# Optimization experiments

Hardware: AMD Instinct MI355X
Metric: run time of the kernel (lower is better)

The kernel has to match this reference:

```python
import jax, jax.numpy as jnp
import numpy as np

D = 256; DFFN = 1024; H = 8; NLVL = 4; NPNT = 4; HD = D // H
BS = 4; NQ = 100; NPTS = 25
SPATIAL = [(128, 128), (64, 64), (32, 32), (16, 16)]
LEN_IN = sum(h * w for h, w in SPATIAL)


def _ln(x, g, b, eps=1e-5):
    m = x.mean(-1, keepdims=True)
    v = ((x - m) ** 2).mean(-1, keepdims=True)
    return (x - m) * jax.lax.rsqrt(v + eps) * g + b


def _mha(q, k, v, w_in, b_in, w_out, b_out):
    # torch nn.MultiheadAttention math, batch-first layout [B,S,D]
    B, Sq, _ = q.shape; Sk = k.shape[1]
    wq, wk, wv = jnp.split(w_in, 3, 0); bq, bk, bv = jnp.split(b_in, 3)
    qh = (q @ wq.T + bq).reshape(B, Sq, H, HD).transpose(0, 2, 1, 3)
    kh = (k @ wk.T + bk).reshape(B, Sk, H, HD).transpose(0, 2, 1, 3)
    vh = (v @ wv.T + bv).reshape(B, Sk, H, HD).transpose(0, 2, 1, 3)
    a = jax.nn.softmax(jnp.einsum('bhqd,bhkd->bhqk', qh, kh) * (1.0 / float(np.sqrt(HD))), -1)
    o = jnp.einsum('bhqk,bhkd->bhqd', a, vh).transpose(0, 2, 1, 3).reshape(B, Sq, D)
    return o @ w_out.T + b_out


def _msdeform(query, ref, src, off_w, off_b, aw_w, aw_b, val_w, val_b, out_w, out_b):
    # MSDeformAttn: per-query multi-level bilinear sampling + weighted aggregation
    bs, Lq, _ = query.shape
    value = (src @ val_w.T + val_b).reshape(bs, LEN_IN, H, HD)
    off = (query @ off_w.T + off_b).reshape(bs, Lq, H, NLVL, NPNT, 2)
    aw = jax.nn.softmax((query @ aw_w.T + aw_b).reshape(bs, Lq, H, NLVL * NPNT), -1)
    aw = aw.reshape(bs, Lq, H, NLVL, NPNT)
    norm = jnp.array([[w, h] for h, w in SPATIAL], jnp.float32)  # (W,H) per level
    loc = ref[:, :, None, :, None, :] + off / norm[None, None, None, :, None, :]
    out = jnp.zeros((bs, H, Lq, HD), query.dtype)
    start = 0
    for l, (hh, ww) in enumerate(SPATIAL):
        v_l = value[:, start:start + hh * ww].transpose(0, 2, 1, 3)  # [bs,H,hw,HD]
        start += hh * ww
        # grid_sample align_corners=False pixel coords: loc*size - 0.5
        x = (loc[:, :, :, l, :, 0] * ww - 0.5).transpose(0, 2, 1, 3).reshape(bs, H, Lq * NPNT)
        y = (loc[:, :, :, l, :, 1] * hh - 0.5).transpose(0, 2, 1, 3).reshape(bs, H, Lq * NPNT)
        x0 = jnp.floor(x); y0 = jnp.floor(y); wx = x - x0; wy = y - y0
        x0i = x0.astype(jnp.int32); y0i = y0.astype(jnp.int32); x1i = x0i + 1; y1i = y0i + 1
        def g(xi, yi):
            valid = ((xi >= 0) & (xi < ww) & (yi >= 0) & (yi < hh)).astype(query.dtype)
            idx = jnp.clip(yi, 0, hh - 1) * ww + jnp.clip(xi, 0, ww - 1)
            return jnp.take_along_axis(v_l, idx[..., None], axis=2) * valid[..., None]
        s = (g(x0i, y0i) * ((1 - wx) * (1 - wy))[..., None]
             + g(x1i, y0i) * (wx * (1 - wy))[..., None]
             + g(x0i, y1i) * ((1 - wx) * wy)[..., None]
             + g(x1i, y1i) * (wx * wy)[..., None])
        s = s.reshape(bs, H, Lq, NPNT, HD)
        out = out + (s * aw[:, :, :, l].transpose(0, 2, 1, 3)[..., None]).sum(3)
    return out.transpose(0, 2, 1, 3).reshape(bs, Lq, D) @ out_w.T + out_b


def _fwd(tgt, query_pos, reference_points, src,
         w_in_intra, b_in_intra, w_out_intra, b_out_intra, g_norm_intra, b_norm_intra,
         w_in_inter, b_in_inter, w_out_inter, b_out_inter, g_norm_inter, b_norm_inter,
         off_w, off_b, aw_w, aw_b, val_w, val_b, co_w, co_b, g_norm_cross, b_norm_cross,
         lin1_w, lin1_b, lin2_w, lin2_b, g_norm3, b_norm3):
    bs, nq, npts, d = tgt.shape
    # intra-instance self-attention (over control points)
    q = (tgt + query_pos).reshape(bs * nq, npts, d)
    t2 = _mha(q, q, tgt.reshape(bs * nq, npts, d), w_in_intra, b_in_intra, w_out_intra, b_out_intra)
    tgt = _ln(tgt + t2.reshape(bs, nq, npts, d), g_norm_intra, b_norm_intra)
    # inter-instance self-attention (over queries), no pos embed per source code
    ti = tgt.transpose(0, 2, 1, 3).reshape(bs * npts, nq, d)
    t2 = _mha(ti, ti, ti, w_in_inter, b_in_inter, w_out_inter, b_out_inter)
    ti = _ln(ti + t2, g_norm_inter, b_norm_inter).reshape(bs, npts, nq, d).transpose(0, 2, 1, 3)
    # deformable cross-attention
    ref = jnp.broadcast_to(reference_points[:, :, None], (bs, nq, npts, NLVL, 2)).reshape(bs, nq * npts, NLVL, 2)
    qc = (ti + query_pos).reshape(bs, nq * npts, d)
    t2 = _msdeform(qc, ref, src, off_w, off_b, aw_w, aw_b, val_w, val_b, co_w, co_b).reshape(bs, nq, npts, d)
    tgt = _ln(ti + t2, g_norm_cross, b_norm_cross)
    # FFN
    ff = jax.nn.relu(tgt @ lin1_w.T + lin1_b) @ lin2_w.T + lin2_b
    return _ln(tgt + ff, g_norm3, b_norm3)


def setup_inputs() -> dict:
    key = jax.random.key(0)
    ki = iter(jax.random.split(key, 40))
    def rn(shape, sc=0.02):
        return jax.random.normal(next(ki), shape, jnp.float32) * sc
    inp = dict(
        tgt=jax.random.normal(next(ki), (BS, NQ, NPTS, D), jnp.float32),
        query_pos=jax.random.normal(next(ki), (BS, NQ, NPTS, D), jnp.float32),
        reference_points=jax.random.uniform(next(ki), (BS, NQ, NLVL, 2), jnp.float32),
        src=jax.random.normal(next(ki), (BS, LEN_IN, D), jnp.float32),
        w_in_intra=rn((3 * D, D)), b_in_intra=jnp.zeros((3 * D,), jnp.float32),
        w_out_intra=rn((D, D)), b_out_intra=jnp.zeros((D,), jnp.float32),
        g_norm_intra=jnp.ones((D,), jnp.float32), b_norm_intra=jnp.zeros((D,), jnp.float32),
        w_in_inter=rn((3 * D, D)), b_in_inter=jnp.zeros((3 * D,), jnp.float32),
        w_out_inter=rn((D, D)), b_out_inter=jnp.zeros((D,), jnp.float32),
        g_norm_inter=jnp.ones((D,), jnp.float32), b_norm_inter=jnp.zeros((D,), jnp.float32),
        off_w=rn((H * NLVL * NPNT * 2, D), 0.001), off_b=rn((H * NLVL * NPNT * 2,), 0.5),
        aw_w=rn((H * NLVL * NPNT, D)), aw_b=jnp.zeros((H * NLVL * NPNT,), jnp.float32),
        val_w=rn((D, D)), val_b=jnp.zeros((D,), jnp.float32),
        co_w=rn((D, D)), co_b=jnp.zeros((D,), jnp.float32),
        g_norm_cross=jnp.ones((D,), jnp.float32), b_norm_cross=jnp.zeros((D,), jnp.float32),
        lin1_w=rn((DFFN, D)), lin1_b=jnp.zeros((DFFN,), jnp.float32),
        lin2_w=rn((D, DFFN)), lin2_b=jnp.zeros((D,), jnp.float32),
        g_norm3=jnp.ones((D,), jnp.float32), b_norm3=jnp.zeros((D,), jnp.float32),
        src_spatial_shapes=jnp.array(SPATIAL, jnp.int32),
        level_start_index=jnp.array(np.cumsum([0] + [h * w for h, w in SPATIAL[:-1]]), jnp.int32),
    )
    return inp


def reference(tgt, query_pos, reference_points, src,
              w_in_intra, b_in_intra, w_out_intra, b_out_intra, g_norm_intra, b_norm_intra,
              w_in_inter, b_in_inter, w_out_inter, b_out_inter, g_norm_inter, b_norm_inter,
              off_w, off_b, aw_w, aw_b, val_w, val_b, co_w, co_b, g_norm_cross, b_norm_cross,
              lin1_w, lin1_b, lin2_w, lin2_b, g_norm3, b_norm3,
              src_spatial_shapes, level_start_index):
    # spatial shapes / level starts are compile-time constants (SPATIAL); args kept for signature parity
    return _fwd(tgt, query_pos, reference_points, src,
                w_in_intra, b_in_intra, w_out_intra, b_out_intra, g_norm_intra, b_norm_intra,
                w_in_inter, b_in_inter, w_out_inter, b_out_inter, g_norm_inter, b_norm_inter,
                off_w, off_b, aw_w, aw_b, val_w, val_b, co_w, co_b, g_norm_cross, b_norm_cross,
                lin1_w, lin1_b, lin2_w, lin2_b, g_norm3, b_norm3)
```

## Files before the change

### kernel.cpp

```cpp
#include <hip/hip_runtime.h>
#include <math.h>

#define DMODEL 256
#define HEADS  8
#define HDIM   32
#define BS     4
#define NQ     100
#define NPTS   25
#define LQ     2500
#define M10K   10000
#define LEN_IN 21760
#define MVAL   87040

typedef float f32x4 __attribute__((ext_vector_type(4)));
typedef short s16x8 __attribute__((ext_vector_type(8)));
typedef unsigned short u16;

static __device__ __forceinline__ short f2bf(float f) {
    unsigned u = __builtin_bit_cast(unsigned, f);
    u = (u + 0x7fffu + ((u >> 16) & 1u)) >> 16;
    return (short)u;
}
static __device__ __forceinline__ unsigned pack2(float lo, float hi) {
    return (unsigned)(u16)f2bf(lo) | ((unsigned)(u16)f2bf(hi) << 16);
}
static __device__ __forceinline__ float bf_lo(unsigned u) {
    return __builtin_bit_cast(float, u << 16);
}
static __device__ __forceinline__ float bf_hi(unsigned u) {
    return __builtin_bit_cast(float, u & 0xffff0000u);
}

#define LDSK 40

__global__ __launch_bounds__(256) void convert_weights_kernel(
    const float* __restrict__ s0, const float* __restrict__ s1,
    const float* __restrict__ s2, const float* __restrict__ s3,
    const float* __restrict__ s4, const float* __restrict__ s5,
    const float* __restrict__ s6, const float* __restrict__ s7,
    const float* __restrict__ s8, const float* __restrict__ s9,
    u16* __restrict__ dst)
{
    int t8 = (blockIdx.x * 256 + threadIdx.x) * 8;
    if (t8 >= 1277952) return;
    const float* s; int base;
    if      (t8 <  196608) { s = s0; base = 0;       }
    else if (t8 <  262144) { s = s1; base = 196608;  }
    else if (t8 <  458752) { s = s2; base = 262144;  }
    else if (t8 <  524288) { s = s3; base = 458752;  }
    else if (t8 <  589824) { s = s4; base = 524288;  }
    else if (t8 <  622592) { s = s5; base = 589824;  }
    else if (t8 <  688128) { s = s6; base = 622592;  }
    else if (t8 <  753664) { s = s7; base = 688128;  }
    else if (t8 < 1015808) { s = s8; base = 753664;  }
    else                   { s = s9; base = 1015808; }
    const float* p = s + (t8 - base);
    float4 a = *(const float4*)p;
    float4 b = *(const float4*)(p + 4);
    s16x8 v;
    v[0]=f2bf(a.x); v[1]=f2bf(a.y); v[2]=f2bf(a.z); v[3]=f2bf(a.w);
    v[4]=f2bf(b.x); v[5]=f2bf(b.y); v[6]=f2bf(b.z); v[7]=f2bf(b.w);
    *(s16x8*)(dst + t8) = v;
}

__global__ __launch_bounds__(256) void add_convert_kernel(
    const float* __restrict__ a, const float* __restrict__ b,
    u16* __restrict__ xb, u16* __restrict__ ab, int n8)
{
    int i = blockIdx.x * 256 + threadIdx.x;
    if (i >= n8) return;
    size_t o = (size_t)i * 8;
    float4 a0 = *(const float4*)(a + o);
    float4 a1 = *(const float4*)(a + o + 4);
    if (ab) {
        s16x8 v;
        v[0]=f2bf(a0.x); v[1]=f2bf(a0.y); v[2]=f2bf(a0.z); v[3]=f2bf(a0.w);
        v[4]=f2bf(a1.x); v[5]=f2bf(a1.y); v[6]=f2bf(a1.z); v[7]=f2bf(a1.w);
        *(s16x8*)(ab + o) = v;
    }
    if (b) {
        float4 b0 = *(const float4*)(b + o);
        float4 b1 = *(const float4*)(b + o + 4);
        a0.x += b0.x; a0.y += b0.y; a0.z += b0.z; a0.w += b0.w;
        a1.x += b1.x; a1.y += b1.y; a1.z += b1.z; a1.w += b1.w;
    }
    s16x8 v;
    v[0]=f2bf(a0.x); v[1]=f2bf(a0.y); v[2]=f2bf(a0.z); v[3]=f2bf(a0.w);
    v[4]=f2bf(a1.x); v[5]=f2bf(a1.y); v[6]=f2bf(a1.z); v[7]=f2bf(a1.w);
    *(s16x8*)(xb + o) = v;
}

__global__ __launch_bounds__(256) void gemm_mfma_kernel(
    const u16* __restrict__ A, int lda,
    const u16* __restrict__ W, int K,
    const float* __restrict__ bias,
    float* __restrict__ C, int ldc, int M)
{
    __shared__ short As[64 * LDSK];
    __shared__ short Ws[64 * LDSK];

    const int tid = threadIdx.x;
    const int m0 = blockIdx.y * 64, n0 = blockIdx.x * 64;
    const int srow = tid >> 2;
    const int skseg = (tid & 3) * 8;
    const int wave = tid >> 6;
    const int wm = wave & 1, wn = wave >> 1;
    const int lane = tid & 63;
    const int lrow = lane & 15;
    const int kq = lane >> 4;

    f32x4 acc[2][2];
#pragma unroll
    for (int i = 0; i < 2; ++i)
#pragma unroll
        for (int j = 0; j < 2; ++j) acc[i][j] = (f32x4)(0.f);

    for (int k0 = 0; k0 < K; k0 += 32) {
        int gm = m0 + srow;
        s16x8 av = (s16x8)0;
        if (gm < M) av = *(const s16x8*)(A + (size_t)gm * lda + k0 + skseg);
        s16x8 wv = *(const s16x8*)(W + (size_t)(n0 + srow) * K + k0 + skseg);
        *(s16x8*)&As[srow * LDSK + skseg] = av;
        *(s16x8*)&Ws[srow * LDSK + skseg] = wv;
        __syncthreads();

        s16x8 af[2], bfv[2];
#pragma unroll
        for (int i = 0; i < 2; ++i)
            af[i] = *(const s16x8*)&As[(wm * 32 + i * 16 + lrow) * LDSK + kq * 8];
#pragma unroll
        for (int j = 0; j < 2; ++j)
            bfv[j] = *(const s16x8*)&Ws[(wn * 32 + j * 16 + lrow) * LDSK + kq * 8];
#pragma unroll
        for (int i = 0; i < 2; ++i)
#pragma unroll
            for (int j = 0; j < 2; ++j)
                acc[i][j] = __builtin_amdgcn_mfma_f32_16x16x32_bf16(af[i], bfv[j], acc[i][j], 0, 0, 0);
        __syncthreads();
    }

#pragma unroll
    for (int i = 0; i < 2; ++i)
#pragma unroll
        for (int j = 0; j < 2; ++j) {
            int col = n0 + wn * 32 + j * 16 + lrow;
            float bv = bias[col];
#pragma unroll
            for (int reg = 0; reg < 4; ++reg) {
                int gm = m0 + wm * 32 + i * 16 + kq * 4 + reg;
                if (gm < M) C[(size_t)gm * ldc + col] = acc[i][j][reg] + bv;
            }
        }
}

__global__ __launch_bounds__(256) void gemm_mfma128_kernel(
    const u16* __restrict__ A, int lda,
    const u16* __restrict__ W, int K,
    const float* __restrict__ bias,
    void* __restrict__ Cv, int ldc,
    int M, int relu, int out_bf16)
{
    __shared__ short As[128 * LDSK];
    __shared__ short Ws[128 * LDSK];

    const int tid = threadIdx.x;
    const int m0 = blockIdx.y * 128, n0 = blockIdx.x * 128;

    const int srow = tid >> 1;
    const int sk = (tid & 1) * 16;

    const int wave = tid >> 6;
    const int wm = wave & 1, wn = wave >> 1;
    const int lane = tid & 63;
    const int lrow = lane & 15;
    const int kq = lane >> 4;

    f32x4 acc[4][4];
#pragma unroll
    for (int i = 0; i < 4; ++i)
#pragma unroll
        for (int j = 0; j < 4; ++j) acc[i][j] = (f32x4)(0.f);

    for (int k0 = 0; k0 < K; k0 += 32) {
        int gm = m0 + srow;
        s16x8 a0 = (s16x8)0, a1 = (s16x8)0;
        if (gm < M) {
            const u16* ap = A + (size_t)gm * lda + k0 + sk;
            a0 = *(const s16x8*)ap;
            a1 = *(const s16x8*)(ap + 8);
        }
        const u16* wp = W + (size_t)(n0 + srow) * K + k0 + sk;
        s16x8 w0 = *(const s16x8*)wp;
        s16x8 w1 = *(const s16x8*)(wp + 8);
        *(s16x8*)&As[srow * LDSK + sk]     = a0;
        *(s16x8*)&As[srow * LDSK + sk + 8] = a1;
        *(s16x8*)&Ws[srow * LDSK + sk]     = w0;
        *(s16x8*)&Ws[srow * LDSK + sk + 8] = w1;
        __syncthreads();

        s16x8 af[4], bfv[4];
#pragma unroll
        for (int i = 0; i < 4; ++i)
            af[i] = *(const s16x8*)&As[(wm * 64 + i * 16 + lrow) * LDSK + kq * 8];
#pragma unroll
        for (int j = 0; j < 4; ++j)
            bfv[j] = *(const s16x8*)&Ws[(wn * 64 + j * 16 + lrow) * LDSK + kq * 8];
#pragma unroll
        for (int i = 0; i < 4; ++i)
#pragma unroll
            for (int j = 0; j < 4; ++j)
                acc[i][j] = __builtin_amdgcn_mfma_f32_16x16x32_bf16(af[i], bfv[j], acc[i][j], 0, 0, 0);
        __syncthreads();
    }

#pragma unroll
    for (int i = 0; i < 4; ++i)
#pragma unroll
        for (int j = 0; j < 4; ++j) {
            int col = n0 + wn * 64 + j * 16 + lrow;
            float bv = bias[col];
#pragma unroll
            for (int reg = 0; reg < 4; ++reg) {
                int gm = m0 + wm * 64 + i * 16 + kq * 4 + reg;
                if (gm < M) {
                    float v = acc[i][j][reg] + bv;
                    if (relu) v = fmaxf(v, 0.f);
                    if (out_bf16)
                        ((u16*)Cv)[(size_t)gm * ldc + col] = (u16)f2bf(v);
                    else
                        ((float*)Cv)[(size_t)gm * ldc + col] = v;
                }
            }
        }
}

__global__ __launch_bounds__(256) void gemm_value_kernel(
    const float* __restrict__ A,
    const u16* __restrict__ W,
    const float* __restrict__ bias,
    u16* __restrict__ C, int M)
{
    __shared__ short As[64 * LDSK];
    __shared__ short Ws[256 * LDSK];

    const int tid = threadIdx.x;
    const int m0 = blockIdx.x * 64;

    const int arow = tid >> 2;
    const int ak = (tid & 3) * 8;

    const int wave = tid >> 6;
    const int lane = tid & 63;
    const int lrow = lane & 15;
    const int kq = lane >> 4;

    f32x4 acc[4][4];
#pragma unroll
    for (int i = 0; i < 4; ++i)
#pragma unroll
        for (int j = 0; j < 4; ++j) acc[i][j] = (f32x4)(0.f);

    for (int k0 = 0; k0 < 256; k0 += 32) {
        int gm = m0 + arow;
        s16x8 av = (s16x8)0;
        if (gm < M) {
            const float* ap = A + (size_t)gm * 256 + k0 + ak;
            float4 a0 = *(const float4*)ap;
            float4 a1 = *(const float4*)(ap + 4);
            av[0]=f2bf(a0.x); av[1]=f2bf(a0.y); av[2]=f2bf(a0.z); av[3]=f2bf(a0.w);
            av[4]=f2bf(a1.x); av[5]=f2bf(a1.y); av[6]=f2bf(a1.z); av[7]=f2bf(a1.w);
        }
        *(s16x8*)&As[arow * LDSK + ak] = av;
#pragma unroll
        for (int it = 0; it < 4; ++it) {
            int n = (tid >> 2) + it * 64;
            s16x8 wv = *(const s16x8*)(W + (size_t)n * 256 + k0 + ak);
            *(s16x8*)&Ws[n * LDSK + ak] = wv;
        }
        __syncthreads();

        s16x8 af[4], bfv[4];
#pragma unroll
        for (int i = 0; i < 4; ++i)
            af[i] = *(const s16x8*)&As[(i * 16 + lrow) * LDSK + kq * 8];
#pragma unroll
        for (int j = 0; j < 4; ++j)
            bfv[j] = *(const s16x8*)&Ws[(wave * 64 + j * 16 + lrow) * LDSK + kq * 8];
#pragma unroll
        for (int i = 0; i < 4; ++i)
#pragma unroll
            for (int j = 0; j < 4; ++j)
                acc[i][j] = __builtin_amdgcn_mfma_f32_16x16x32_bf16(af[i], bfv[j], acc[i][j], 0, 0, 0);
        __syncthreads();
    }

#pragma unroll
    for (int i = 0; i < 4; ++i)
#pragma unroll
        for (int j = 0; j < 4; ++j) {
            int col = wave * 64 + j * 16 + lrow;
            float bv = bias[col];
#pragma unroll
            for (int reg = 0; reg < 4; ++reg) {
                int gm = m0 + i * 16 + kq * 4 + reg;
                if (gm < M)
                    C[(size_t)gm * 256 + col] = (u16)f2bf(acc[i][j][reg] + bv);
            }
        }
}

__global__ __launch_bounds__(512) void inter_attn_kernel(
    const float* __restrict__ qkv, u16* __restrict__ out, float scale)
{
    __shared__ float4 Kv[100][16];
    __shared__ float4 Ml4[100];
    __shared__ float4 Ll4[100];
    __shared__ float  O[100][33];

    const int b = blockIdx.x, h = blockIdx.y;
    const float* base = qkv + (size_t)b * 100 * 768;
    const int tid = threadIdx.x;
    const int r = tid & 127, kc = tid >> 7;

    for (int idx = tid; idx < 1600; idx += 512) {
        int row = idx >> 4, seg = idx & 15;
        const float* src = (seg < 8)
            ? base + row * 768 + 256 + h * 32 + seg * 4
            : base + row * 768 + 512 + h * 32 + (seg - 8) * 4;
        Kv[row][seg] = *(const float4*)src;
    }
    for (int idx = tid; idx < 100 * 33; idx += 512)
        ((float*)O)[idx] = 0.f;

    float q[32];
    if (r < 100) {
        const float* qp = base + r * 768 + h * 32;
#pragma unroll
        for (int c4 = 0; c4 < 8; ++c4) {
            float4 f = *(const float4*)(qp + c4 * 4);
            q[c4*4+0] = f.x; q[c4*4+1] = f.y; q[c4*4+2] = f.z; q[c4*4+3] = f.w;
        }
    }
    __syncthreads();

    float m = -1e30f, l = 0.f, acc[32];
#pragma unroll
    for (int c = 0; c < 32; ++c) acc[c] = 0.f;

    if (r < 100) {
        const int j0 = kc * 25;
#pragma unroll 2
        for (int s = 0; s < 25; ++s) {
            const float4* kr = &Kv[j0 + s][0];
            float dot = 0.f;
#pragma unroll
            for (int c4 = 0; c4 < 8; ++c4) {
                float4 kf = kr[c4];
                dot = fmaf(q[c4*4+0], kf.x, dot);
                dot = fmaf(q[c4*4+1], kf.y, dot);
                dot = fmaf(q[c4*4+2], kf.z, dot);
                dot = fmaf(q[c4*4+3], kf.w, dot);
            }
            dot *= scale;
            float mn = fmaxf(m, dot);
            float alpha = __expf(m - mn);
            float p = __expf(dot - mn);
            l = l * alpha + p;
            const float4* vr = &Kv[j0 + s][8];
#pragma unroll
            for (int c4 = 0; c4 < 8; ++c4) {
                float4 vf = vr[c4];
                acc[c4*4+0] = acc[c4*4+0] * alpha + p * vf.x;
                acc[c4*4+1] = acc[c4*4+1] * alpha + p * vf.y;
                acc[c4*4+2] = acc[c4*4+2] * alpha + p * vf.z;
                acc[c4*4+3] = acc[c4*4+3] * alpha + p * vf.w;
            }
            m = mn;
        }
        ((float*)&Ml4[r])[kc] = m;
        ((float*)&Ll4[r])[kc] = l;
    }
    __syncthreads();

    float alphaK = 0.f, Ltot = 1.f;
    if (r < 100) {
        float4 mv = Ml4[r];
        float4 lv = Ll4[r];
        float M = fmaxf(fmaxf(mv.x, mv.y), fmaxf(mv.z, mv.w));
        Ltot = __expf(mv.x - M) * lv.x + __expf(mv.y - M) * lv.y
             + __expf(mv.z - M) * lv.z + __expf(mv.w - M) * lv.w;
        alphaK = __expf(m - M);
    }
    for (int cc = 0; cc < 4; ++cc) {
        if (kc == cc && r < 100) {
#pragma unroll
            for (int c = 0; c < 32; ++c) O[r][c] += alphaK * acc[c];
        }
        __syncthreads();
    }
    if (kc == 0 && r < 100) {
        float inv = 1.f / Ltot;
        unsigned* op = (unsigned*)(out + ((size_t)b * 100 + r) * 256 + h * 32);
#pragma unroll
        for (int c = 0; c < 16; ++c)
            op[c] = pack2(O[r][2*c] * inv, O[r][2*c+1] * inv);
    }
}

__global__ __launch_bounds__(256) void intra_attn_kernel(
    const float* __restrict__ qkv, u16* __restrict__ out, float scale)
{
    __shared__ float4 KV[25][128];

    const int b = blockIdx.x;
    const int h = threadIdx.x >> 5, r = threadIdx.x & 31;
    const float* base = qkv + (size_t)b * 25 * 768;

    for (int idx = threadIdx.x; idx < 3200; idx += 256) {
        int row = idx >> 7, c = idx & 127;
        KV[row][c] = *(const float4*)(base + row * 768 + 256 + c * 4);
    }

    float q[32];
    if (r < 25) {
        const float* qp = base + r * 768 + h * 32;
#pragma unroll
        for (int c4 = 0; c4 < 8; ++c4) {
            float4 f = *(const float4*)(qp + c4 * 4);
            q[c4*4+0] = f.x; q[c4*4+1] = f.y; q[c4*4+2] = f.z; q[c4*4+3] = f.w;
        }
    }
    __syncthreads();

    if (r < 25) {
        float m = -1e30f, l = 0.f, acc[32];
#pragma unroll
        for (int c = 0; c < 32; ++c) acc[c] = 0.f;
#pragma unroll 2
        for (int j = 0; j < 25; ++j) {
            const float4* kr = &KV[j][h * 8];
            float dot = 0.f;
#pragma unroll
            for (int c4 = 0; c4 < 8; ++c4) {
                float4 kf = kr[c4];
                dot = fmaf(q[c4*4+0], kf.x, dot);
                dot = fmaf(q[c4*4+1], kf.y, dot);
                dot = fmaf(q[c4*4+2], kf.z, dot);
                dot = fmaf(q[c4*4+3], kf.w, dot);
            }
            dot *= scale;
            float mn = fmaxf(m, dot);
            float alpha = __expf(m - mn);
            float p = __expf(dot - mn);
            l = l * alpha + p;
            const float4* vr = &KV[j][64 + h * 8];
#pragma unroll
            for (int c4 = 0; c4 < 8; ++c4) {
                float4 vf = vr[c4];
                acc[c4*4+0] = acc[c4*4+0] * alpha + p * vf.x;
                acc[c4*4+1] = acc[c4*4+1] * alpha + p * vf.y;
                acc[c4*4+2] = acc[c4*4+2] * alpha + p * vf.z;
                acc[c4*4+3] = acc[c4*4+3] * alpha + p * vf.w;
            }
            m = mn;
        }
        float inv = 1.f / l;
        unsigned* op = (unsigned*)(out + ((size_t)b * 25 + r) * 256 + h * 32);
#pragma unroll
        for (int c = 0; c < 16; ++c)
            op[c] = pack2(acc[2*c] * inv, acc[2*c+1] * inv);
    }
}

__global__ __launch_bounds__(64) void add_ln_kernel(
    const float* __restrict__ a, const float* __restrict__ b,
    const float* __restrict__ g, const float* __restrict__ beta,
    float* __restrict__ out, u16* __restrict__ out_bf, int transpose_mode)
{
    const int r = blockIdx.x;
    const int lane = threadIdx.x;
    const float* ar = a + (size_t)r * 256;
    const float* br = b + (size_t)r * 256;
    float x[4];
    float s = 0.f;
#pragma unroll
    for (int i = 0; i < 4; ++i) {
        x[i] = ar[lane + 64 * i] + br[lane + 64 * i];
        s += x[i];
    }
#pragma unroll
    for (int off = 32; off >= 1; off >>= 1) s += __shfl_xor(s, off);
    float mean = s * (1.f / 256.f);
    float vs = 0.f;
#pragma unroll
    for (int i = 0; i < 4; ++i) { float d = x[i] - mean; vs += d * d; }
#pragma unroll
    for (int off = 32; off >= 1; off >>= 1) vs += __shfl_xor(vs, off);
    float rstd = rsqrtf(vs * (1.f / 256.f) + 1e-5f);

    size_t ro = r;
    if (transpose_mode) {
        int q = r % 100; int bp = r / 100; int p = bp % 25; int bb = bp / 25;
        ro = ((size_t)bb * 100 + q) * 25 + p;
    }
    float* orow = out + ro * 256;
    u16* brow = out_bf ? out_bf + ro * 256 : (u16*)0;
#pragma unroll
    for (int i = 0; i < 4; ++i) {
        int c = lane + 64 * i;
        float v = (x[i] - mean) * rstd * g[c] + beta[c];
        orow[c] = v;
        if (brow) brow[c] = (u16)f2bf(v);
    }
}

__global__ __launch_bounds__(64) void tgt_to_ti_kernel(
    const float* __restrict__ tgt1, float* __restrict__ ti, u16* __restrict__ tib)
{
    const int r = blockIdx.x;
    int q = r % 100; int bp = r / 100; int p = bp % 25; int b = bp / 25;
    const float4* srcp = (const float4*)(tgt1 + (((size_t)b * 100 + q) * 25 + p) * 256);
    float4 v = srcp[threadIdx.x];
    ((float4*)(ti + (size_t)r * 256))[threadIdx.x] = v;
    uint2 pk = make_uint2(pack2(v.x, v.y), pack2(v.z, v.w));
    ((uint2*)(tib + (size_t)r * 256))[threadIdx.x] = pk;
}

__global__ __launch_bounds__(256, 4) void msdeform_sample_kernel(
    const u16* __restrict__ value,
    const float* __restrict__ off,
    const float* __restrict__ awl,
    const float* __restrict__ refp,
    u16* __restrict__ sampled)
{
    const int unit = blockIdx.x * 8 + (threadIdx.x >> 5);
    const int t = threadIdx.x & 31;
    const int h = t >> 2, c8 = t & 3;
    const int b = unit / LQ, lq = unit - b * LQ;
    const int q = lq / NPTS;

    const float* awp = awl + (size_t)unit * 128 + h * 16;
    float w[16];
    float mx = -1e30f;
#pragma unroll
    for (int k = 0; k < 16; ++k) { w[k] = awp[k]; mx = fmaxf(mx, w[k]); }
    float sum = 0.f;
#pragma unroll
    for (int k = 0; k < 16; ++k) { w[k] = __expf(w[k] - mx); sum += w[k]; }
    const float inv = 1.f / sum;

    const float* offp = off + (size_t)unit * 256 + h * 32;
    const float* rp = refp + ((size_t)b * 100 + q) * 8;
    const u16* vbase = value + (size_t)b * LEN_IN * 256 + h * 32 + c8 * 8;

    float acc[8];
#pragma unroll
    for (int k = 0; k < 8; ++k) acc[k] = 0.f;

    int start = 0;
    const int sz[4] = {128, 64, 32, 16};
#pragma unroll
    for (int l = 0; l < 4; ++l) {
        const int hh = sz[l], ww = sz[l];
        const float rx = rp[l * 2 + 0], ry = rp[l * 2 + 1];
#pragma unroll 1
        for (int pt = 0; pt < 4; ++pt) {
            float ox = offp[(l * 4 + pt) * 2 + 0];
            float oy = offp[(l * 4 + pt) * 2 + 1];
            float x = rx * ww + ox - 0.5f;
            float y = ry * hh + oy - 0.5f;
            float x0f = floorf(x), y0f = floorf(y);
            float wx = x - x0f, wy = y - y0f;
            int x0 = (int)x0f, y0 = (int)y0f;
            int x1 = x0 + 1, y1 = y0 + 1;
            float aw = w[l * 4 + pt] * inv;

            int x0c = min(max(x0, 0), ww - 1), x1c = min(max(x1, 0), ww - 1);
            int y0c = min(max(y0, 0), hh - 1), y1c = min(max(y1, 0), hh - 1);
            float w00 = aw * (1.f - wx) * (1.f - wy);
            float w10 = aw * wx * (1.f - wy);
            float w01 = aw * (1.f - wx) * wy;
            float w11 = aw * wx * wy;
            if (!(x0 >= 0 && x0 < ww)) { w00 = 0.f; w01 = 0.f; }
            if (!(x1 >= 0 && x1 < ww)) { w10 = 0.f; w11 = 0.f; }
            if (!(y0 >= 0 && y0 < hh)) { w00 = 0.f; w10 = 0.f; }
            if (!(y1 >= 0 && y1 < hh)) { w01 = 0.f; w11 = 0.f; }

            uint4 u00 = *(const uint4*)(vbase + (size_t)(start + y0c * ww + x0c) * 256);
            uint4 u10 = *(const uint4*)(vbase + (size_t)(start + y0c * ww + x1c) * 256);
            uint4 u01 = *(const uint4*)(vbase + (size_t)(start + y1c * ww + x0c) * 256);
            uint4 u11 = *(const uint4*)(vbase + (size_t)(start + y1c * ww + x1c) * 256);

#define ACC4(u, wgt) \
            acc[0] = fmaf(wgt, bf_lo(u.x), acc[0]); \
            acc[1] = fmaf(wgt, bf_hi(u.x), acc[1]); \
            acc[2] = fmaf(wgt, bf_lo(u.y), acc[2]); \
            acc[3] = fmaf(wgt, bf_hi(u.y), acc[3]); \
            acc[4] = fmaf(wgt, bf_lo(u.z), acc[4]); \
            acc[5] = fmaf(wgt, bf_hi(u.z), acc[5]); \
            acc[6] = fmaf(wgt, bf_lo(u.w), acc[6]); \
            acc[7] = fmaf(wgt, bf_hi(u.w), acc[7]);
            ACC4(u00, w00); ACC4(u10, w10); ACC4(u01, w01); ACC4(u11, w11);
#undef ACC4
        }
        start += hh * ww;
    }

    uint4 pk;
    pk.x = pack2(acc[0], acc[1]); pk.y = pack2(acc[2], acc[3]);
    pk.z = pack2(acc[4], acc[5]); pk.w = pack2(acc[6], acc[7]);
    *(uint4*)(sampled + (size_t)unit * 256 + h * 32 + c8 * 8) = pk;
}

extern "C" void kernel_launch(void* const* d_in, const int* in_sizes, int n_in,
                              void* d_out, int out_size, void* d_ws, size_t ws_size,
                              hipStream_t stream)
{
    (void)in_sizes; (void)n_in; (void)out_size; (void)ws_size;

    const float* tgt        = (const float*)d_in[0];
    const float* query_pos  = (const float*)d_in[1];
    const float* refp       = (const float*)d_in[2];
    const float* src        = (const float*)d_in[3];
    const float* w_in_intra = (const float*)d_in[4];
    const float* b_in_intra = (const float*)d_in[5];
    const float* w_out_intra= (const float*)d_in[6];
    const float* b_out_intra= (const float*)d_in[7];
    const float* g_ln_intra = (const float*)d_in[8];
    const float* b_ln_intra = (const float*)d_in[9];
    const float* w_in_inter = (const float*)d_in[10];
    const float* b_in_inter = (const float*)d_in[11];
    const float* w_out_inter= (const float*)d_in[12];
    const float* b_out_inter= (const float*)d_in[13];
    const float* g_ln_inter = (const float*)d_in[14];
    const float* b_ln_inter = (const float*)d_in[15];
    const float* off_w      = (const float*)d_in[16];
    const float* off_b      = (const float*)d_in[17];
    const float* aw_w       = (const float*)d_in[18];
    const float* aw_b       = (const float*)d_in[19];
    const float* val_w      = (const float*)d_in[20];
    const float* val_b      = (const float*)d_in[21];
    const float* co_w       = (const float*)d_in[22];
    const float* co_b       = (const float*)d_in[23];
    const float* g_ln_cross = (const float*)d_in[24];
    const float* b_ln_cross = (const float*)d_in[25];
    const float* lin1_w     = (const float*)d_in[26];
    const float* lin1_b     = (const float*)d_in[27];
    const float* lin2_w     = (const float*)d_in[28];
    const float* lin2_b     = (const float*)d_in[29];
    const float* g_ln3      = (const float*)d_in[30];
    const float* b_ln3      = (const float*)d_in[31];

    float* ws    = (float*)d_ws;
    float* qkv   = ws;
    float* tmp   = ws + 7680000;
    u16*   attnb = (u16*)(ws + 10240000);
    float* tgt1  = ws + 11520000;
    float* ti    = ws + 14080000;
    u16*   tib   = (u16*)(ws + 16640000);
    float* tA    = ws + 17920000;
    u16*   qcb   = (u16*)(ws + 20480000);
    u16*   x1b   = (u16*)(ws + 21760000);
    u16*   tgtb  = (u16*)(ws + 23040000);
    float* awl   = ws + 24320000;
    u16*   valueb= (u16*)(ws + 25600000);
    u16*   wb    = (u16*)(ws + 36741120);
    float* out   = (float*)d_out;

    u16* wb_in_intra  = wb;
    u16* wb_out_intra = wb + 196608;
    u16* wb_in_inter  = wb + 262144;
    u16* wb_out_inter = wb + 458752;
    u16* wb_off       = wb + 524288;
    u16* wb_aw        = wb + 589824;
    u16* wb_val       = wb + 622592;
    u16* wb_co        = wb + 688128;
    u16* wb_lin1      = wb + 753664;
    u16* wb_lin2      = wb + 1015808;

    const float scale = 0.17677669529663687f;
    const int MB128 = (M10K + 127) / 128;

    convert_weights_kernel<<<624, 256, 0, stream>>>(
        w_in_intra, w_out_intra, w_in_inter, w_out_inter, off_w,
        aw_w, val_w, co_w, lin1_w, lin2_w, wb);
    add_convert_kernel<<<1250, 256, 0, stream>>>(tgt, query_pos, x1b, tgtb, 320000);

    gemm_mfma128_kernel<<<dim3(4, MB128), 256, 0, stream>>>(x1b, 256, wb_in_intra, 256,
                                                            b_in_intra, qkv, 768, M10K, 0, 0);
    gemm_mfma128_kernel<<<dim3(2, MB128), 256, 0, stream>>>(tgtb, 256, wb_in_intra + 512 * 256, 256,
                                                            b_in_intra + 512, qkv + 512, 768, M10K, 0, 0);
    intra_attn_kernel<<<400, 256, 0, stream>>>(qkv, attnb, scale);
    gemm_mfma128_kernel<<<dim3(2, MB128), 256, 0, stream>>>(attnb, 256, wb_out_intra, 256,
                                                            b_out_intra, tmp, 256, M10K, 0, 0);
    add_ln_kernel<<<M10K, 64, 0, stream>>>(tgt, tmp, g_ln_intra, b_ln_intra, tgt1, (u16*)0, 0);

    tgt_to_ti_kernel<<<M10K, 64, 0, stream>>>(tgt1, ti, tib);
    gemm_mfma128_kernel<<<dim3(6, MB128), 256, 0, stream>>>(tib, 256, wb_in_inter, 256,
                                                            b_in_inter, qkv, 768, M10K, 0, 0);
    inter_attn_kernel<<<dim3(100, 8), 512, 0, stream>>>(qkv, attnb, scale);
    gemm_mfma128_kernel<<<dim3(2, MB128), 256, 0, stream>>>(attnb, 256, wb_out_inter, 256,
                                                            b_out_inter, tmp, 256, M10K, 0, 0);
    add_ln_kernel<<<M10K, 64, 0, stream>>>(ti, tmp, g_ln_inter, b_ln_inter, tA, (u16*)0, 1);

    add_convert_kernel<<<1250, 256, 0, stream>>>(tA, query_pos, qcb, (u16*)0, 320000);
    gemm_value_kernel<<<1360, 256, 0, stream>>>(src, wb_val, val_b, valueb, MVAL);
    gemm_mfma128_kernel<<<dim3(2, MB128), 256, 0, stream>>>(qcb, 256, wb_off, 256,
                                                            off_b, tgt1, 256, M10K, 0, 0);
    gemm_mfma_kernel<<<dim3(2, 157), 256, 0, stream>>>(qcb, 256, wb_aw, 256,
                                                       aw_b, awl, 128, M10K);
    msdeform_sample_kernel<<<1250, 256, 0, stream>>>(valueb, tgt1, awl, refp, attnb);
    gemm_mfma128_kernel<<<dim3(2, MB128), 256, 0, stream>>>(attnb, 256, wb_co, 256,
                                                            co_b, tmp, 256, M10K, 0, 0);
    add_ln_kernel<<<M10K, 64, 0, stream>>>(tA, tmp, g_ln_cross, b_ln_cross, ti, tib, 0);

    gemm_mfma128_kernel<<<dim3(8, MB128), 256, 0, stream>>>(tib, 256, wb_lin1, 256,
                                                            lin1_b, valueb, 1024, M10K, 1, 1);
    gemm_mfma128_kernel<<<dim3(2, MB128), 256, 0, stream>>>(valueb, 1024, wb_lin2, 1024,
                                                            lin2_b, tmp, 256, M10K, 0, 0);
    add_ln_kernel<<<M10K, 64, 0, stream>>>(ti, tmp, g_ln3, b_ln3, out, (u16*)0, 0);
}
```

Baseline: 548.0 us.

## Prefetch GEMM tiles to registers, use MFMA inter-attention, smaller tiles for N=256

Adds register double-buffering to all three GEMM kernels, so the global loads for the next K-slice are issued after the barrier and overlap with the MFMA work on the current slice. Replaces the scalar FP32 online-softmax inter-attention kernel with a bf16 MFMA version that computes QK^T, softmax and PV through padded LDS tiles. Switches the N=256 GEMMs from 128x128 to 64x64 tiles to launch more blocks. This gives more parallelism at the cost of extra register pressure and lower per-block reuse, and attention probabilities are now rounded to bf16.

```diff
diff --git a/kernel.cpp b/kernel.cpp
--- a/kernel.cpp
+++ b/kernel.cpp
@@ -94,7 +94,8 @@
     const u16* __restrict__ A, int lda,
     const u16* __restrict__ W, int K,
     const float* __restrict__ bias,
-    float* __restrict__ C, int ldc, int M)
+    void* __restrict__ Cv, int ldc,
+    int M, int relu, int out_bf16)
 {
     __shared__ short As[64 * LDSK];
     __shared__ short Ws[64 * LDSK];
@@ -109,20 +110,28 @@
     const int lrow = lane & 15;
     const int kq = lane >> 4;
 
+    const int gm = m0 + srow;
+    const u16* aptr = A + (size_t)gm * lda + skseg;
+    const u16* wptr = W + (size_t)(n0 + srow) * K + skseg;
+
     f32x4 acc[2][2];
 #pragma unroll
     for (int i = 0; i < 2; ++i)
 #pragma unroll
         for (int j = 0; j < 2; ++j) acc[i][j] = (f32x4)(0.f);
 
+    s16x8 avr = (s16x8)0, wvr;
+    if (gm < M) avr = *(const s16x8*)aptr;
+    wvr = *(const s16x8*)wptr;
+
     for (int k0 = 0; k0 < K; k0 += 32) {
-        int gm = m0 + srow;
-        s16x8 av = (s16x8)0;
-        if (gm < M) av = *(const s16x8*)(A + (size_t)gm * lda + k0 + skseg);
-        s16x8 wv = *(const s16x8*)(W + (size_t)(n0 + srow) * K + k0 + skseg);
-        *(s16x8*)&As[srow * LDSK + skseg] = av;
-        *(s16x8*)&Ws[srow * LDSK + skseg] = wv;
+        *(s16x8*)&As[srow * LDSK + skseg] = avr;
+        *(s16x8*)&Ws[srow * LDSK + skseg] = wvr;
         __syncthreads();
+        if (k0 + 32 < K) {
+            if (gm < M) avr = *(const s16x8*)(aptr + k0 + 32);
+            wvr = *(const s16x8*)(wptr + k0 + 32);
+        }
 
         s16x8 af[2], bfv[2];
 #pragma unroll
@@ -147,8 +156,15 @@
             float bv = bias[col];
 #pragma unroll
             for (int reg = 0; reg < 4; ++reg) {
-                int gm = m0 + wm * 32 + i * 16 + kq * 4 + reg;
-                if (gm < M) C[(size_t)gm * ldc + col] = acc[i][j][reg] + bv;
+                int gmo = m0 + wm * 32 + i * 16 + kq * 4 + reg;
+                if (gmo < M) {
+                    float v = acc[i][j][reg] + bv;
+                    if (relu) v = fmaxf(v, 0.f);
+                    if (out_bf16)
+                        ((u16*)Cv)[(size_t)gmo * ldc + col] = (u16)f2bf(v);
+                    else
+                        ((float*)Cv)[(size_t)gmo * ldc + col] = v;
+                }
             }
         }
 }
@@ -175,28 +191,34 @@
     const int lrow = lane & 15;
     const int kq = lane >> 4;
 
+    const int gm = m0 + srow;
+    const u16* aptr = A + (size_t)gm * lda + sk;
+    const u16* wptr = W + (size_t)(n0 + srow) * K + sk;
+
     f32x4 acc[4][4];
 #pragma unroll
     for (int i = 0; i < 4; ++i)
 #pragma unroll
         for (int j = 0; j < 4; ++j) acc[i][j] = (f32x4)(0.f);
 
+    s16x8 a0 = (s16x8)0, a1 = (s16x8)0, w0, w1;
+    if (gm < M) { a0 = *(const s16x8*)aptr; a1 = *(const s16x8*)(aptr + 8); }
+    w0 = *(const s16x8*)wptr; w1 = *(const s16x8*)(wptr + 8);
+
     for (int k0 = 0; k0 < K; k0 += 32) {
-        int gm = m0 + srow;
-        s16x8 a0 = (s16x8)0, a1 = (s16x8)0;
-        if (gm < M) {
-            const u16* ap = A + (size_t)gm * lda + k0 + sk;
-            a0 = *(const s16x8*)ap;
-            a1 = *(const s16x8*)(ap + 8);
-        }
-        const u16* wp = W + (size_t)(n0 + srow) * K + k0 + sk;
-        s16x8 w0 = *(const s16x8*)wp;
-        s16x8 w1 = *(const s16x8*)(wp + 8);
         *(s16x8*)&As[srow * LDSK + sk]     = a0;
         *(s16x8*)&As[srow * LDSK + sk + 8] = a1;
         *(s16x8*)&Ws[srow * LDSK + sk]     = w0;
         *(s16x8*)&Ws[srow * LDSK + sk + 8] = w1;
         __syncthreads();
+        if (k0 + 32 < K) {
+            if (gm < M) {
+                a0 = *(const s16x8*)(aptr + k0 + 32);
+                a1 = *(const s16x8*)(aptr + k0 + 40);
+            }
+            w0 = *(const s16x8*)(wptr + k0 + 32);
+            w1 = *(const s16x8*)(wptr + k0 + 40);
+        }
 
         s16x8 af[4], bfv[4];
 #pragma unroll
@@ -221,14 +243,14 @@
             float bv = bias[col];
 #pragma unroll
             for (int reg = 0; reg < 4; ++reg) {
-                int gm = m0 + wm * 64 + i * 16 + kq * 4 + reg;
-                if (gm < M) {
+                int gmo = m0 + wm * 64 + i * 16 + kq * 4 + reg;
+                if (gmo < M) {
                     float v = acc[i][j][reg] + bv;
                     if (relu) v = fmaxf(v, 0.f);
                     if (out_bf16)
-                        ((u16*)Cv)[(size_t)gm * ldc + col] = (u16)f2bf(v);
+                        ((u16*)Cv)[(size_t)gmo * ldc + col] = (u16)f2bf(v);
                     else
-                        ((float*)Cv)[(size_t)gm * ldc + col] = v;
+                        ((float*)Cv)[(size_t)gmo * ldc + col] = v;
                 }
             }
         }
@@ -254,30 +276,40 @@
     const int lrow = lane & 15;
     const int kq = lane >> 4;
 
+    const int gm = m0 + arow;
+    const float* aptr = A + (size_t)gm * 256 + ak;
+
     f32x4 acc[4][4];
 #pragma unroll
     for (int i = 0; i < 4; ++i)
 #pragma unroll
         for (int j = 0; j < 4; ++j) acc[i][j] = (f32x4)(0.f);
 
+    float4 pa0 = make_float4(0.f,0.f,0.f,0.f), pa1 = pa0;
+    if (gm < M) { pa0 = *(const float4*)aptr; pa1 = *(const float4*)(aptr + 4); }
+    s16x8 pw[4];
+#pragma unroll
+    for (int it = 0; it < 4; ++it)
+        pw[it] = *(const s16x8*)(W + (size_t)((tid >> 2) + it * 64) * 256 + ak);
+
     for (int k0 = 0; k0 < 256; k0 += 32) {
-        int gm = m0 + arow;
-        s16x8 av = (s16x8)0;
-        if (gm < M) {
-            const float* ap = A + (size_t)gm * 256 + k0 + ak;
-            float4 a0 = *(const float4*)ap;
-            float4 a1 = *(const float4*)(ap + 4);
-            av[0]=f2bf(a0.x); av[1]=f2bf(a0.y); av[2]=f2bf(a0.z); av[3]=f2bf(a0.w);
-            av[4]=f2bf(a1.x); av[5]=f2bf(a1.y); av[6]=f2bf(a1.z); av[7]=f2bf(a1.w);
-        }
+        s16x8 av;
+        av[0]=f2bf(pa0.x); av[1]=f2bf(pa0.y); av[2]=f2bf(pa0.z); av[3]=f2bf(pa0.w);
+        av[4]=f2bf(pa1.x); av[5]=f2bf(pa1.y); av[6]=f2bf(pa1.z); av[7]=f2bf(pa1.w);
         *(s16x8*)&As[arow * LDSK + ak] = av;
 #pragma unroll
-        for (int it = 0; it < 4; ++it) {
-            int n = (tid >> 2) + it * 64;
-            s16x8 wv = *(const s16x8*)(W + (size_t)n * 256 + k0 + ak);
-            *(s16x8*)&Ws[n * LDSK + ak] = wv;
-        }
+        for (int it = 0; it < 4; ++it)
+            *(s16x8*)&Ws[((tid >> 2) + it * 64) * LDSK + ak] = pw[it];
         __syncthreads();
+        if (k0 + 32 < 256) {
+            if (gm < M) {
+                pa0 = *(const float4*)(aptr + k0 + 32);
+                pa1 = *(const float4*)(aptr + k0 + 36);
+            }
+#pragma unroll
+            for (int it = 0; it < 4; ++it)
+                pw[it] = *(const s16x8*)(W + (size_t)((tid >> 2) + it * 64) * 256 + k0 + 32 + ak);
+        }
 
         s16x8 af[4], bfv[4];
 #pragma unroll
@@ -302,108 +334,123 @@
             float bv = bias[col];
 #pragma unroll
             for (int reg = 0; reg < 4; ++reg) {
-                int gm = m0 + i * 16 + kq * 4 + reg;
-                if (gm < M)
-                    C[(size_t)gm * 256 + col] = (u16)f2bf(acc[i][j][reg] + bv);
-            }
-        }
-}
-
-__global__ __launch_bounds__(512) void inter_attn_kernel(
+                int gmo = m0 + i * 16 + kq * 4 + reg;
+                if (gmo < M)
+                    C[(size_t)gmo * 256 + col] = (u16)f2bf(acc[i][j][reg] + bv);
+            }
+        }
+}
+
+__global__ __launch_bounds__(256) void inter_attn_mfma_kernel(
     const float* __restrict__ qkv, u16* __restrict__ out, float scale)
 {
-    __shared__ float4 Kv[100][16];
-    __shared__ float4 Ml4[100];
-    __shared__ float4 Ll4[100];
-    __shared__ float  O[100][33];
+    __shared__ __align__(16) u16 Qs[112 * 40];
+    __shared__ __align__(16) u16 Ks[112 * 40];
+    __shared__ __align__(16) u16 Vt[32 * 136];
+    __shared__ __align__(16) u16 Ps[112 * 136];
 
     const int b = blockIdx.x, h = blockIdx.y;
     const float* base = qkv + (size_t)b * 100 * 768;
     const int tid = threadIdx.x;
-    const int r = tid & 127, kc = tid >> 7;
-
-    for (int idx = tid; idx < 1600; idx += 512) {
-        int row = idx >> 4, seg = idx & 15;
-        const float* src = (seg < 8)
-            ? base + row * 768 + 256 + h * 32 + seg * 4
-            : base + row * 768 + 512 + h * 32 + (seg - 8) * 4;
-        Kv[row][seg] = *(const float4*)src;
-    }
-    for (int idx = tid; idx < 100 * 33; idx += 512)
-        ((float*)O)[idx] = 0.f;
-
-    float q[32];
-    if (r < 100) {
-        const float* qp = base + r * 768 + h * 32;
-#pragma unroll
-        for (int c4 = 0; c4 < 8; ++c4) {
-            float4 f = *(const float4*)(qp + c4 * 4);
-            q[c4*4+0] = f.x; q[c4*4+1] = f.y; q[c4*4+2] = f.z; q[c4*4+3] = f.w;
-        }
-    }
+    const int wave = tid >> 6, lane = tid & 63;
+    const int lr = lane & 15, quad = lane >> 4;
+
+    for (int i = tid; i < 12 * 20; i += 256) {
+        int row = 100 + i / 20, c = (i % 20) * 2;
+        *(unsigned*)&Qs[row * 40 + c] = 0;
+        *(unsigned*)&Ks[row * 40 + c] = 0;
+    }
+    for (int i = tid; i < 2176; i += 256) ((unsigned*)Vt)[i] = 0;
+    for (int i = tid; i < 7616; i += 256) ((unsigned*)Ps)[i] = 0;
     __syncthreads();
 
-    float m = -1e30f, l = 0.f, acc[32];
-#pragma unroll
-    for (int c = 0; c < 32; ++c) acc[c] = 0.f;
-
-    if (r < 100) {
-        const int j0 = kc * 25;
-#pragma unroll 2
-        for (int s = 0; s < 25; ++s) {
-            const float4* kr = &Kv[j0 + s][0];
-            float dot = 0.f;
-#pragma unroll
-            for (int c4 = 0; c4 < 8; ++c4) {
-                float4 kf = kr[c4];
-                dot = fmaf(q[c4*4+0], kf.x, dot);
-                dot = fmaf(q[c4*4+1], kf.y, dot);
-                dot = fmaf(q[c4*4+2], kf.z, dot);
-                dot = fmaf(q[c4*4+3], kf.w, dot);
-            }
-            dot *= scale;
-            float mn = fmaxf(m, dot);
-            float alpha = __expf(m - mn);
-            float p = __expf(dot - mn);
-            l = l * alpha + p;
-            const float4* vr = &Kv[j0 + s][8];
-#pragma unroll
-            for (int c4 = 0; c4 < 8; ++c4) {
-                float4 vf = vr[c4];
-                acc[c4*4+0] = acc[c4*4+0] * alpha + p * vf.x;
-                acc[c4*4+1] = acc[c4*4+1] * alpha + p * vf.y;
-                acc[c4*4+2] = acc[c4*4+2] * alpha + p * vf.z;
-                acc[c4*4+3] = acc[c4*4+3] * alpha + p * vf.w;
-            }
-            m = mn;
-        }
-        ((float*)&Ml4[r])[kc] = m;
-        ((float*)&Ll4[r])[kc] = l;
+    for (int idx = tid; idx < 2400; idx += 256) {
+        int row = idx / 24, s = idx % 24;
+        const float* p = (s < 8)  ? base + row * 768 + h * 32 + s * 4
+                       : (s < 16) ? base + row * 768 + 256 + h * 32 + (s - 8) * 4
+                                  : base + row * 768 + 512 + h * 32 + (s - 16) * 4;
+        float4 f = *(const float4*)p;
+        if (s < 8) {
+            unsigned* q = (unsigned*)&Qs[row * 40 + s * 4];
+            q[0] = pack2(f.x, f.y); q[1] = pack2(f.z, f.w);
+        } else if (s < 16) {
+            unsigned* q = (unsigned*)&Ks[row * 40 + (s - 8) * 4];
+            q[0] = pack2(f.x, f.y); q[1] = pack2(f.z, f.w);
+        } else {
+            int d0 = (s - 16) * 4;
+            Vt[(d0 + 0) * 136 + row] = (u16)f2bf(f.x);
+            Vt[(d0 + 1) * 136 + row] = (u16)f2bf(f.y);
+            Vt[(d0 + 2) * 136 + row] = (u16)f2bf(f.z);
+            Vt[(d0 + 3) * 136 + row] = (u16)f2bf(f.w);
+        }
     }
     __syncthreads();
 
-    float alphaK = 0.f, Ltot = 1.f;
-    if (r < 100) {
-        float4 mv = Ml4[r];
-        float4 lv = Ll4[r];
-        float M = fmaxf(fmaxf(mv.x, mv.y), fmaxf(mv.z, mv.w));
-        Ltot = __expf(mv.x - M) * lv.x + __expf(mv.y - M) * lv.y
-             + __expf(mv.z - M) * lv.z + __expf(mv.w - M) * lv.w;
-        alphaK = __expf(m - M);
-    }
-    for (int cc = 0; cc < 4; ++cc) {
-        if (kc == cc && r < 100) {
-#pragma unroll
-            for (int c = 0; c < 32; ++c) O[r][c] += alphaK * acc[c];
-        }
-        __syncthreads();
-    }
-    if (kc == 0 && r < 100) {
-        float inv = 1.f / Ltot;
-        unsigned* op = (unsigned*)(out + ((size_t)b * 100 + r) * 256 + h * 32);
-#pragma unroll
-        for (int c = 0; c < 16; ++c)
-            op[c] = pack2(O[r][2*c] * inv, O[r][2*c+1] * inv);
+#pragma unroll 1
+    for (int rr = 0; rr < 2; ++rr) {
+        int rt = wave + rr * 4;
+        if (rt < 7) {
+            s16x8 aq = *(const s16x8*)&Qs[(rt * 16 + lr) * 40 + quad * 8];
+            f32x4 sc[7];
+#pragma unroll
+            for (int ct = 0; ct < 7; ++ct) {
+                s16x8 bk = *(const s16x8*)&Ks[(ct * 16 + lr) * 40 + quad * 8];
+                sc[ct] = __builtin_amdgcn_mfma_f32_16x16x32_bf16(aq, bk, (f32x4)(0.f), 0, 0, 0);
+            }
+            const bool colok[7] = {true, true, true, true, true, true, (lr < 4)};
+#pragma unroll
+            for (int reg = 0; reg < 4; ++reg) {
+                float mx = -1e30f;
+#pragma unroll
+                for (int ct = 0; ct < 7; ++ct) {
+                    float sv = sc[ct][reg] * scale;
+                    sc[ct][reg] = sv;
+                    if (colok[ct]) mx = fmaxf(mx, sv);
+                }
+#pragma unroll
+                for (int d = 1; d < 16; d <<= 1) mx = fmaxf(mx, __shfl_xor(mx, d));
+                float ssum = 0.f;
+#pragma unroll
+                for (int ct = 0; ct < 7; ++ct) {
+                    float pv = colok[ct] ? __expf(sc[ct][reg] - mx) : 0.f;
+                    sc[ct][reg] = pv;
+                    ssum += pv;
+                }
+#pragma unroll
+                for (int d = 1; d < 16; d <<= 1) ssum += __shfl_xor(ssum, d);
+                float inv = 1.f / ssum;
+                int prow = rt * 16 + quad * 4 + reg;
+#pragma unroll
+                for (int ct = 0; ct < 7; ++ct)
+                    Ps[prow * 136 + ct * 16 + lr] = (u16)f2bf(sc[ct][reg] * inv);
+            }
+        }
+    }
+    __syncthreads();
+
+#pragma unroll 1
+    for (int rr = 0; rr < 2; ++rr) {
+        int rt = wave + rr * 4;
+        if (rt < 7) {
+            f32x4 o0 = (f32x4)(0.f), o1 = (f32x4)(0.f);
+#pragma unroll
+            for (int kk = 0; kk < 4; ++kk) {
+                s16x8 ap = *(const s16x8*)&Ps[(rt * 16 + lr) * 136 + kk * 32 + quad * 8];
+                s16x8 bv0 = *(const s16x8*)&Vt[lr * 136 + kk * 32 + quad * 8];
+                s16x8 bv1 = *(const s16x8*)&Vt[(16 + lr) * 136 + kk * 32 + quad * 8];
+                o0 = __builtin_amdgcn_mfma_f32_16x16x32_bf16(ap, bv0, o0, 0, 0, 0);
+                o1 = __builtin_amdgcn_mfma_f32_16x16x32_bf16(ap, bv1, o1, 0, 0, 0);
+            }
+#pragma unroll
+            for (int reg = 0; reg < 4; ++reg) {
+                int q = rt * 16 + quad * 4 + reg;
+                if (q < 100) {
+                    u16* op = out + ((size_t)b * 100 + q) * 256 + h * 32;
+                    op[lr]      = (u16)f2bf(o0[reg]);
+                    op[16 + lr] = (u16)f2bf(o1[reg]);
+                }
+            }
+        }
     }
 }
 
@@ -679,6 +726,7 @@
     u16* wb_lin2      = wb + 1015808;
 
     const float scale = 0.17677669529663687f;
+    const int MB64  = (M10K + 63) / 64;
     const int MB128 = (M10K + 127) / 128;
 
     convert_weights_kernel<<<624, 256, 0, stream>>>(
@@ -688,35 +736,35 @@
 
     gemm_mfma128_kernel<<<dim3(4, MB128), 256, 0, stream>>>(x1b, 256, wb_in_intra, 256,
                                                             b_in_intra, qkv, 768, M10K, 0, 0);
-    gemm_mfma128_kernel<<<dim3(2, MB128), 256, 0, stream>>>(tgtb, 256, wb_in_intra + 512 * 256, 256,
-                                                            b_in_intra + 512, qkv + 512, 768, M10K, 0, 0);
+    gemm_mfma_kernel<<<dim3(4, MB64), 256, 0, stream>>>(tgtb, 256, wb_in_intra + 512 * 256, 256,
+                                                        b_in_intra + 512, qkv + 512, 768, M10K, 0, 0);
     intra_attn_kernel<<<400, 256, 0, stream>>>(qkv, attnb, scale);
-    gemm_mfma128_kernel<<<dim3(2, MB128), 256, 0, stream>>>(attnb, 256, wb_out_intra, 256,
-                                                            b_out_intra, tmp, 256, M10K, 0, 0);
+    gemm_mfma_kernel<<<dim3(4, MB64), 256, 0, stream>>>(attnb, 256, wb_out_intra, 256,
+                                                        b_out_intra, tmp, 256, M10K, 0, 0);
     add_ln_kernel<<<M10K, 64, 0, stream>>>(tgt, tmp, g_ln_intra, b_ln_intra, tgt1, (u16*)0, 0);
 
     tgt_to_ti_kernel<<<M10K, 64, 0, stream>>>(tgt1, ti, tib);
     gemm_mfma128_kernel<<<dim3(6, MB128), 256, 0, stream>>>(tib, 256, wb_in_inter, 256,
                                                             b_in_inter, qkv, 768, M10K, 0, 0);
-    inter_attn_kernel<<<dim3(100, 8), 512, 0, stream>>>(qkv, attnb, scale);
-    gemm_mfma128_kernel<<<dim3(2, MB128), 256, 0, stream>>>(attnb, 256, wb_out_inter, 256,
-                                                            b_out_inter, tmp, 256, M10K, 0, 0);
+    inter_attn_mfma_kernel<<<dim3(100, 8), 256, 0, stream>>>(qkv, attnb, scale);
+    gemm_mfma_kernel<<<dim3(4, MB64), 256, 0, stream>>>(attnb, 256, wb_out_inter, 256,
+                                                        b_out_inter, tmp, 256, M10K, 0, 0);
     add_ln_kernel<<<M10K, 64, 0, stream>>>(ti, tmp, g_ln_inter, b_ln_inter, tA, (u16*)0, 1);
 
     add_convert_kernel<<<1250, 256, 0, stream>>>(tA, query_pos, qcb, (u16*)0, 320000);
     gemm_value_kernel<<<1360, 256, 0, stream>>>(src, wb_val, val_b, valueb, MVAL);
-    gemm_mfma128_kernel<<<dim3(2, MB128), 256, 0, stream>>>(qcb, 256, wb_off, 256,
-                                                            off_b, tgt1, 256, M10K, 0, 0);
-    gemm_mfma_kernel<<<dim3(2, 157), 256, 0, stream>>>(qcb, 256, wb_aw, 256,
-                                                       aw_b, awl, 128, M10K);
+    gemm_mfma_kernel<<<dim3(4, MB64), 256, 0, stream>>>(qcb, 256, wb_off, 256,
+                                                        off_b, tgt1, 256, M10K, 0, 0);
+    gemm_mfma_kernel<<<dim3(2, MB64), 256, 0, stream>>>(qcb, 256, wb_aw, 256,
+                                                        aw_b, awl, 128, M10K, 0, 0);
     msdeform_sample_kernel<<<1250, 256, 0, stream>>>(valueb, tgt1, awl, refp, attnb);
-    gemm_mfma128_kernel<<<dim3(2, MB128), 256, 0, stream>>>(attnb, 256, wb_co, 256,
-                                                            co_b, tmp, 256, M10K, 0, 0);
+    gemm_mfma_kernel<<<dim3(4, MB64), 256, 0, stream>>>(attnb, 256, wb_co, 256,
+                                                        co_b, tmp, 256, M10K, 0, 0);
     add_ln_kernel<<<M10K, 64, 0, stream>>>(tA, tmp, g_ln_cross, b_ln_cross, ti, tib, 0);
 
     gemm_mfma128_kernel<<<dim3(8, MB128), 256, 0, stream>>>(tib, 256, wb_lin1, 256,
                                                             lin1_b, valueb, 1024, M10K, 1, 1);
-    gemm_mfma128_kernel<<<dim3(2, MB128), 256, 0, stream>>>(valueb, 1024, wb_lin2, 1024,
-                                                            lin2_b, tmp, 256, M10K, 0, 0);
+    gemm_mfma_kernel<<<dim3(4, MB64), 256, 0, stream>>>(valueb, 1024, wb_lin2, 1024,
+                                                        lin2_b, tmp, 256, M10K, 0, 0);
     add_ln_kernel<<<M10K, 64, 0, stream>>>(ti, tmp, g_ln3, b_ln3, out, (u16*)0, 0);
 }
```

Result: faster. 472.8 us (-13.7%).
